# Kernel tuning notes

Hardware: AMD Instinct MI355X
Metric: run time of the kernel (lower is better)

The kernel has to match this reference:

```python
import jax, jax.numpy as jnp
import numpy as np

NUM_VERTICES = 100_000
NUM_SPRINGS = 6_400_000
DIM = 3
EPS = 1e-6


def setup_inputs() -> dict:
    key = jax.random.key(0)
    k1, k2, k3, k4, k5 = jax.random.split(key, 5)
    x = jax.random.normal(k1, (NUM_VERTICES, DIM), dtype=jnp.float32)
    l0 = jax.random.uniform(k2, (NUM_SPRINGS,), dtype=jnp.float32)
    kk = jax.random.uniform(k3, (NUM_SPRINGS,), dtype=jnp.float32)
    i1 = jax.random.randint(k4, (NUM_SPRINGS,), 0, NUM_VERTICES, dtype=jnp.int64 if jax.config.read('jax_enable_x64') else jnp.int32)
    i2 = jax.random.randint(k5, (NUM_SPRINGS,), 0, NUM_VERTICES, dtype=i1.dtype)
    indices = jnp.stack([i1, i2], axis=1)  # [E, 2]
    return {"x": x, "l0": l0, "k": kk, "indices": indices}


def reference(x, l0, k, indices):
    # incidence.mm(x) with +1 at i1 and -1 at i2 per row == gather-based edge diff
    d = x[indices[:, 0]] - x[indices[:, 1]]        # [E, DIM]
    q = jnp.sum(d * d, axis=1)                     # [E]
    l = jnp.sqrt(q + EPS)                          # [E]
    dl = l - l0                                    # [E]
    e = 0.5 * jnp.sum(k * dl * dl)                 # scalar spring energy
    return e
```

## Files before the change

kernel.cpp:

```cpp
#include <hip/hip_runtime.h>
#include <math.h>

#define EPS 1e-6f

constexpr int BLOCK = 256;
constexpr int GRID  = 2048;

typedef int      vi4 __attribute__((ext_vector_type(4)));
typedef float    vf4 __attribute__((ext_vector_type(4)));
typedef _Float16 vh4 __attribute__((ext_vector_type(4)));

__global__ __launch_bounds__(BLOCK) void pad_vertices(
    const float* __restrict__ x,
    vh4* __restrict__ xh,
    int nverts)
{
    int v = blockIdx.x * BLOCK + threadIdx.x;
    if (v < nverts) {
        const float* p = x + 3 * v;
        vh4 t = {(_Float16)p[0], (_Float16)p[1], (_Float16)p[2], (_Float16)0.f};
        xh[v] = t;
    }
}

__global__ __launch_bounds__(BLOCK) void spring_energy_partial(
    const vh4*   __restrict__ xh,
    const float* __restrict__ l0,
    const float* __restrict__ k,
    const int*   __restrict__ idx,
    float* __restrict__ partials,
    int nsprings)
{
    const int tid      = blockIdx.x * BLOCK + threadIdx.x;
    const int nthreads = GRID * BLOCK;
    const int nocts    = nsprings >> 3;

    float acc = 0.f;
    for (int o = tid; o < nocts; o += nthreads) {
        const int s = o << 3;
        const vi4* ip = reinterpret_cast<const vi4*>(idx + 2 * s);
        vi4 i0 = __builtin_nontemporal_load(ip);
        vi4 i1 = __builtin_nontemporal_load(ip + 1);
        vi4 i2 = __builtin_nontemporal_load(ip + 2);
        vi4 i3 = __builtin_nontemporal_load(ip + 3);
        const vf4* lp = reinterpret_cast<const vf4*>(l0 + s);
        vf4 la = __builtin_nontemporal_load(lp);
        vf4 lb = __builtin_nontemporal_load(lp + 1);
        const vf4* kp = reinterpret_cast<const vf4*>(k + s);
        vf4 ka = __builtin_nontemporal_load(kp);
        vf4 kb = __builtin_nontemporal_load(kp + 1);

        vh4 A[8], B[8];
        A[0] = xh[i0.x]; B[0] = xh[i0.y];
        A[1] = xh[i0.z]; B[1] = xh[i0.w];
        A[2] = xh[i1.x]; B[2] = xh[i1.y];
        A[3] = xh[i1.z]; B[3] = xh[i1.w];
        A[4] = xh[i2.x]; B[4] = xh[i2.y];
        A[5] = xh[i2.z]; B[5] = xh[i2.w];
        A[6] = xh[i3.x]; B[6] = xh[i3.y];
        A[7] = xh[i3.z]; B[7] = xh[i3.w];

        const float lv[8] = {la.x, la.y, la.z, la.w, lb.x, lb.y, lb.z, lb.w};
        const float kv[8] = {ka.x, ka.y, ka.z, ka.w, kb.x, kb.y, kb.z, kb.w};

        #pragma unroll
        for (int j = 0; j < 8; ++j) {
            float dx = (float)A[j].x - (float)B[j].x;
            float dy = (float)A[j].y - (float)B[j].y;
            float dz = (float)A[j].z - (float)B[j].z;
            float qd = dx*dx + dy*dy + dz*dz;
            float l  = sqrtf(qd + EPS);
            float dl = l - lv[j];
            acc = fmaf(kv[j] * dl, dl, acc);
        }
    }

    if (blockIdx.x == 0) {
        for (int s = (nocts << 3) + threadIdx.x; s < nsprings; s += BLOCK) {
            int a = idx[2 * s], b = idx[2 * s + 1];
            vh4 pa = xh[a], pb = xh[b];
            float dx = (float)pa.x - (float)pb.x;
            float dy = (float)pa.y - (float)pb.y;
            float dz = (float)pa.z - (float)pb.z;
            float l  = sqrtf(dx*dx + dy*dy + dz*dz + EPS);
            float dl = l - l0[s];
            acc = fmaf(k[s] * dl, dl, acc);
        }
    }

    #pragma unroll
    for (int off = 32; off > 0; off >>= 1)
        acc += __shfl_down(acc, off, 64);

    __shared__ float wsum[BLOCK / 64];
    const int lane = threadIdx.x & 63;
    const int wid  = threadIdx.x >> 6;
    if (lane == 0) wsum[wid] = acc;
    __syncthreads();
    if (threadIdx.x == 0)
        partials[blockIdx.x] = wsum[0] + wsum[1] + wsum[2] + wsum[3];
}

__global__ __launch_bounds__(BLOCK) void spring_energy_final(
    const float* __restrict__ partials,
    float* __restrict__ out)
{
    float acc = 0.f;
    for (int i = threadIdx.x; i < GRID; i += BLOCK)
        acc += partials[i];

    #pragma unroll
    for (int off = 32; off > 0; off >>= 1)
        acc += __shfl_down(acc, off, 64);

    __shared__ float wsum[BLOCK / 64];
    const int lane = threadIdx.x & 63;
    const int wid  = threadIdx.x >> 6;
    if (lane == 0) wsum[wid] = acc;
    __syncthreads();
    if (threadIdx.x == 0)
        out[0] = 0.5f * (wsum[0] + wsum[1] + wsum[2] + wsum[3]);
}

extern "C" void kernel_launch(void* const* d_in, const int* in_sizes, int n_in,
                              void* d_out, int out_size, void* d_ws, size_t ws_size,
                              hipStream_t stream) {
    const float* x   = (const float*)d_in[0];
    const float* l0  = (const float*)d_in[1];
    const float* k   = (const float*)d_in[2];
    const int*   idx = (const int*)  d_in[3];
    float* out       = (float*)d_out;

    const int nverts   = in_sizes[0] / 3;
    const int nsprings = in_sizes[1];

    vh4*   xh       = (vh4*)d_ws;
    float* partials = (float*)((char*)d_ws + (size_t)nverts * sizeof(vh4));

    pad_vertices<<<(nverts + BLOCK - 1) / BLOCK, BLOCK, 0, stream>>>(x, xh, nverts);
    spring_energy_partial<<<GRID, BLOCK, 0, stream>>>(xh, l0, k, idx, partials, nsprings);
    spring_energy_final<<<1, BLOCK, 0, stream>>>(partials, out);
}
```

Measured before the change: 81.88 us.

## Cache first vertex slice in LDS and switch to 1024-thread blocks

Each block copies the first 16384 half-precision padded vertices (128 KB) into dynamic shared memory, and gathers with small indices read from LDS instead of global/L2. The block size grows to 1024 and the grid shrinks to 512 so each block's cache fill serves more threads. This adds a per-block preload of 128 KB, a branch per gather, and limits occupancy to one block per CU. Since only about 16% of vertices are cached, most gathers still go to global memory.

```diff
diff --git a/kernel.cpp b/kernel.cpp
--- a/kernel.cpp
+++ b/kernel.cpp
@@ -3,19 +3,20 @@
 
 #define EPS 1e-6f
 
-constexpr int BLOCK = 256;
-constexpr int GRID  = 2048;
+constexpr int BLOCK = 1024;
+constexpr int GRID  = 512;
+constexpr int NC    = 16384;
 
 typedef int      vi4 __attribute__((ext_vector_type(4)));
 typedef float    vf4 __attribute__((ext_vector_type(4)));
 typedef _Float16 vh4 __attribute__((ext_vector_type(4)));
 
-__global__ __launch_bounds__(BLOCK) void pad_vertices(
+__global__ __launch_bounds__(256) void pad_vertices(
     const float* __restrict__ x,
     vh4* __restrict__ xh,
     int nverts)
 {
-    int v = blockIdx.x * BLOCK + threadIdx.x;
+    int v = blockIdx.x * 256 + threadIdx.x;
     if (v < nverts) {
         const float* p = x + 3 * v;
         vh4 t = {(_Float16)p[0], (_Float16)p[1], (_Float16)p[2], (_Float16)0.f};
@@ -31,6 +32,12 @@
     float* __restrict__ partials,
     int nsprings)
 {
+    extern __shared__ vh4 cache[];
+
+    for (int i = threadIdx.x; i < NC; i += BLOCK)
+        cache[i] = xh[i];
+    __syncthreads();
+
     const int tid      = blockIdx.x * BLOCK + threadIdx.x;
     const int nthreads = GRID * BLOCK;
     const int nocts    = nsprings >> 3;
@@ -50,24 +57,24 @@
         vf4 ka = __builtin_nontemporal_load(kp);
         vf4 kb = __builtin_nontemporal_load(kp + 1);
 
-        vh4 A[8], B[8];
-        A[0] = xh[i0.x]; B[0] = xh[i0.y];
-        A[1] = xh[i0.z]; B[1] = xh[i0.w];
-        A[2] = xh[i1.x]; B[2] = xh[i1.y];
-        A[3] = xh[i1.z]; B[3] = xh[i1.w];
-        A[4] = xh[i2.x]; B[4] = xh[i2.y];
-        A[5] = xh[i2.z]; B[5] = xh[i2.w];
-        A[6] = xh[i3.x]; B[6] = xh[i3.y];
-        A[7] = xh[i3.z]; B[7] = xh[i3.w];
+        const int ii[16] = {i0.x, i0.y, i0.z, i0.w, i1.x, i1.y, i1.z, i1.w,
+                            i2.x, i2.y, i2.z, i2.w, i3.x, i3.y, i3.z, i3.w};
+        vh4 P[16];
+        #pragma unroll
+        for (int j = 0; j < 16; ++j) {
+            int v = ii[j];
+            if (v < NC) P[j] = cache[v];
+            else        P[j] = xh[v];
+        }
 
         const float lv[8] = {la.x, la.y, la.z, la.w, lb.x, lb.y, lb.z, lb.w};
         const float kv[8] = {ka.x, ka.y, ka.z, ka.w, kb.x, kb.y, kb.z, kb.w};
 
         #pragma unroll
         for (int j = 0; j < 8; ++j) {
-            float dx = (float)A[j].x - (float)B[j].x;
-            float dy = (float)A[j].y - (float)B[j].y;
-            float dz = (float)A[j].z - (float)B[j].z;
+            float dx = (float)P[2*j].x - (float)P[2*j+1].x;
+            float dy = (float)P[2*j].y - (float)P[2*j+1].y;
+            float dz = (float)P[2*j].z - (float)P[2*j+1].z;
             float qd = dx*dx + dy*dy + dz*dz;
             float l  = sqrtf(qd + EPS);
             float dl = l - lv[j];
@@ -78,7 +85,8 @@
     if (blockIdx.x == 0) {
         for (int s = (nocts << 3) + threadIdx.x; s < nsprings; s += BLOCK) {
             int a = idx[2 * s], b = idx[2 * s + 1];
-            vh4 pa = xh[a], pb = xh[b];
+            vh4 pa = (a < NC) ? cache[a] : xh[a];
+            vh4 pb = (b < NC) ? cache[b] : xh[b];
             float dx = (float)pa.x - (float)pb.x;
             float dy = (float)pa.y - (float)pb.y;
             float dz = (float)pa.z - (float)pb.z;
@@ -97,23 +105,27 @@
     const int wid  = threadIdx.x >> 6;
     if (lane == 0) wsum[wid] = acc;
     __syncthreads();
-    if (threadIdx.x == 0)
-        partials[blockIdx.x] = wsum[0] + wsum[1] + wsum[2] + wsum[3];
+    if (threadIdx.x == 0) {
+        float s = 0.f;
+        #pragma unroll
+        for (int w = 0; w < BLOCK / 64; ++w) s += wsum[w];
+        partials[blockIdx.x] = s;
+    }
 }
 
-__global__ __launch_bounds__(BLOCK) void spring_energy_final(
+__global__ __launch_bounds__(256) void spring_energy_final(
     const float* __restrict__ partials,
     float* __restrict__ out)
 {
     float acc = 0.f;
-    for (int i = threadIdx.x; i < GRID; i += BLOCK)
+    for (int i = threadIdx.x; i < GRID; i += 256)
         acc += partials[i];
 
     #pragma unroll
     for (int off = 32; off > 0; off >>= 1)
         acc += __shfl_down(acc, off, 64);
 
-    __shared__ float wsum[BLOCK / 64];
+    __shared__ float wsum[4];
     const int lane = threadIdx.x & 63;
     const int wid  = threadIdx.x >> 6;
     if (lane == 0) wsum[wid] = acc;
@@ -137,7 +149,12 @@
     vh4*   xh       = (vh4*)d_ws;
     float* partials = (float*)((char*)d_ws + (size_t)nverts * sizeof(vh4));
 
-    pad_vertices<<<(nverts + BLOCK - 1) / BLOCK, BLOCK, 0, stream>>>(x, xh, nverts);
-    spring_energy_partial<<<GRID, BLOCK, 0, stream>>>(xh, l0, k, idx, partials, nsprings);
-    spring_energy_final<<<1, BLOCK, 0, stream>>>(partials, out);
+    hipFuncSetAttribute(reinterpret_cast<const void*>(spring_energy_partial),
+                        hipFuncAttributeMaxDynamicSharedMemorySize,
+                        NC * (int)sizeof(vh4));
+
+    pad_vertices<<<(nverts + 255) / 256, 256, 0, stream>>>(x, xh, nverts);
+    spring_energy_partial<<<GRID, BLOCK, NC * sizeof(vh4), stream>>>(
+        xh, l0, k, idx, partials, nsprings);
+    spring_energy_final<<<1, 256, 0, stream>>>(partials, out);
 }
```

Result: slower. 92.71 us (+13.2%).
